# Performance work log

Measured on AMD Instinct MI355X. Metric: run time of the kernel, lower is better.

## Reference

```python
import jax, jax.numpy as jnp
import numpy as np

N_NODES = 50000
N_EDGES = 1600000
NODE_DIM = 1024
HID = 128
OUT = 128
LN_EPS = 1e-5


def setup_inputs() -> dict:
    key = jax.random.key(0)
    ks = jax.random.split(key, 8)
    s = lambda d: 1.0 / np.sqrt(d)
    return {
        "x": jax.random.normal(ks[0], (N_NODES, NODE_DIM), jnp.float32),
        "edge_index": jax.random.randint(ks[1], (2, N_EDGES), 0, N_NODES, jnp.int64),
        "proj_w": jax.random.normal(ks[2], (HID, NODE_DIM), jnp.float32) * s(NODE_DIM),
        "proj_b": jnp.zeros((HID,), jnp.float32),
        "lin_l_w": jax.random.normal(ks[3], (HID, HID), jnp.float32) * s(HID),
        "lin_l_b": jnp.zeros((HID,), jnp.float32),
        "lin_r_w": jax.random.normal(ks[4], (HID, HID), jnp.float32) * s(HID),
        "ln_g": jnp.ones((HID,), jnp.float32),
        "ln_b": jnp.zeros((HID,), jnp.float32),
        "out_w": jax.random.normal(ks[5], (OUT, HID), jnp.float32) * s(HID),
        "out_b": jnp.zeros((OUT,), jnp.float32),
    }


def reference(x, edge_index, proj_w, proj_b, lin_l_w, lin_l_b, lin_r_w, ln_g, ln_b, out_w, out_b):
    n = x.shape[0]
    # input projection + ReLU: [N, node_dim] -> [N, H]
    h = jax.nn.relu(x @ proj_w.T + proj_b)
    # SAGEConv(mean): gather source features, mean-scatter to targets
    src, dst = edge_index[0], edge_index[1]
    agg = jax.ops.segment_sum(h[src], dst, num_segments=n)  # [N, H]
    deg = jax.ops.segment_sum(jnp.ones((src.shape[0],), h.dtype), dst, num_segments=n)
    mean_nbr = agg / jnp.maximum(deg, 1.0)[:, None]
    h = mean_nbr @ lin_l_w.T + lin_l_b + h @ lin_r_w.T
    # LayerNorm over feature dim
    mu = h.mean(-1, keepdims=True)
    var = jnp.mean((h - mu) ** 2, -1, keepdims=True)
    h = (h - mu) * jax.lax.rsqrt(var + LN_EPS) * ln_g + ln_b
    h = jax.nn.relu(h)  # dropout is identity in eval
    # batch=None -> global mean pool over all nodes: [1, H]
    g = h.mean(0, keepdims=True)
    return g @ out_w.T + out_b
```

## Files before the change

kernel.cpp:

```cpp
#include <hip/hip_runtime.h>

#define N_NODES  50000
#define N_EDGES  1600000
#define NODE_DIM 1024
#define HID      128
#define LN_EPS   1e-5f
#define NBUCK    196
#define SHARD    6250

typedef float f32x4 __attribute__((ext_vector_type(4)));
typedef __bf16 bf16x8 __attribute__((ext_vector_type(8)));
typedef unsigned short u16x8 __attribute__((ext_vector_type(8)));
typedef unsigned int u32x4 __attribute__((ext_vector_type(4)));

__device__ __forceinline__ unsigned short f2bf(float f) {
  __bf16 b = (__bf16)f;
  return __builtin_bit_cast(unsigned short, b);
}
__device__ __forceinline__ unsigned int pkbf(float a, float b) {
  return (unsigned int)f2bf(a) | ((unsigned int)f2bf(b) << 16);
}
__device__ __forceinline__ float bf2f(unsigned short v) {
  return __uint_as_float((unsigned int)v << 16);
}

__device__ __forceinline__ int scan256_excl(int v, int buf[2][256], int t) {
  int cur = 0;
  buf[0][t] = v;
  __syncthreads();
  for (int off = 1; off < 256; off <<= 1) {
    int nxt = cur ^ 1;
    int s = buf[cur][t];
    if (t >= off) s += buf[cur][t - off];
    buf[nxt][t] = s;
    cur = nxt;
    __syncthreads();
  }
  return buf[cur][t] - v;
}

__global__ __launch_bounds__(256) void k_wpack(const float* __restrict__ w,
                                               unsigned short* __restrict__ wp) {
  int idx = blockIdx.x * 256 + threadIdx.x;
  int lane = idx & 63;
  int n = (idx >> 6) & 7;
  int ks = idx >> 9;
  int fr = lane & 15, kg = lane >> 4;
  const float* src = w + (size_t)(n * 16 + fr) * NODE_DIM + ks * 32 + kg * 8;
  float4 v0 = *(const float4*)(src);
  float4 v1 = *(const float4*)(src + 4);
  unsigned int* o = (unsigned int*)(wp + (size_t)idx * 8);
  o[0] = pkbf(v0.x, v0.y);
  o[1] = pkbf(v0.z, v0.w);
  o[2] = pkbf(v1.x, v1.y);
  o[3] = pkbf(v1.z, v1.w);
}

__global__ __launch_bounds__(256, 3) void k_proj(const float* __restrict__ x,
                                                 const unsigned short* __restrict__ wp,
                                                 const float* __restrict__ pb,
                                                 unsigned short* __restrict__ h) {
  const int wave = threadIdx.x >> 6, lane = threadIdx.x & 63;
  const int fr = lane & 15, kg = lane >> 4;
  const int strip = blockIdx.x * 4 + wave;
  const int m0 = strip * 32;

  int r0 = m0 + fr;      if (r0 >= N_NODES) r0 = N_NODES - 1;
  int r1 = m0 + 16 + fr; if (r1 >= N_NODES) r1 = N_NODES - 1;
  const float* a0p = x + (size_t)r0 * NODE_DIM + kg * 8;
  const float* a1p = x + (size_t)r1 * NODE_DIM + kg * 8;
  const bf16x8* bp = (const bf16x8*)wp + lane;

  f32x4 acc[2][8] = {};

  float4 xa0, xa1, xa2, xa3;
  float4 ya0, ya1, ya2, ya3;

#define LOADA_X(KS) { const float* p0 = a0p + (KS) * 32; const float* p1 = a1p + (KS) * 32; \
  xa0 = *(const float4*)p0; xa1 = *(const float4*)(p0 + 4); \
  xa2 = *(const float4*)p1; xa3 = *(const float4*)(p1 + 4); }
#define LOADA_Y(KS) { const float* p0 = a0p + (KS) * 32; const float* p1 = a1p + (KS) * 32; \
  ya0 = *(const float4*)p0; ya1 = *(const float4*)(p0 + 4); \
  ya2 = *(const float4*)p1; ya3 = *(const float4*)(p1 + 4); }

#define COMPUTE(A0, A1, A2, A3, KS) { \
  bf16x8 bfv[8]; \
  _Pragma("unroll") \
  for (int n = 0; n < 8; n++) bfv[n] = bp[((KS) * 8 + n) * 64]; \
  u32x4 pa0, pa1; \
  pa0[0] = pkbf(A0.x, A0.y); pa0[1] = pkbf(A0.z, A0.w); \
  pa0[2] = pkbf(A1.x, A1.y); pa0[3] = pkbf(A1.z, A1.w); \
  pa1[0] = pkbf(A2.x, A2.y); pa1[1] = pkbf(A2.z, A2.w); \
  pa1[2] = pkbf(A3.x, A3.y); pa1[3] = pkbf(A3.z, A3.w); \
  bf16x8 af0 = __builtin_bit_cast(bf16x8, pa0); \
  bf16x8 af1 = __builtin_bit_cast(bf16x8, pa1); \
  _Pragma("unroll") \
  for (int n = 0; n < 8; n++) { \
    acc[0][n] = __builtin_amdgcn_mfma_f32_16x16x32_bf16(af0, bfv[n], acc[0][n], 0, 0, 0); \
    acc[1][n] = __builtin_amdgcn_mfma_f32_16x16x32_bf16(af1, bfv[n], acc[1][n], 0, 0, 0); \
  } }

  LOADA_X(0);
  for (int ks = 0; ks < 32; ks += 2) {
    LOADA_Y(ks + 1);
    COMPUTE(xa0, xa1, xa2, xa3, ks);
    if (ks + 2 < 32) LOADA_X(ks + 2);
    COMPUTE(ya0, ya1, ya2, ya3, ks + 1);
  }
#undef LOADA_X
#undef LOADA_Y
#undef COMPUTE

  const int cr = (lane >> 4) * 4, cc = lane & 15;
#pragma unroll
  for (int n = 0; n < 8; n++) {
    const int col = n * 16 + cc;
    const float bias = pb[col];
#pragma unroll
    for (int m = 0; m < 2; m++) {
      const int rowb = m0 + m * 16 + cr;
#pragma unroll
      for (int i = 0; i < 4; i++) {
        float v = acc[m][n][i] + bias;
        h[(size_t)(rowb + i) * HID + col] = f2bf(v > 0.f ? v : 0.f);
      }
    }
  }
}

__global__ __launch_bounds__(256) void k_hist(const int* __restrict__ ei,
                                              int* __restrict__ counts) {
  __shared__ int bins[NBUCK];
  int t = threadIdx.x;
  if (t < NBUCK) bins[t] = 0;
  __syncthreads();
  int base = blockIdx.x * SHARD;
  for (int i = t; i < SHARD; i += 256)
    atomicAdd(&bins[ei[N_EDGES + base + i] >> 8], 1);
  __syncthreads();
  if (t < NBUCK) counts[t * 256 + blockIdx.x] = bins[t];
}

__global__ __launch_bounds__(256) void k_s1(const int* __restrict__ counts,
                                            int* __restrict__ basem,
                                            int* __restrict__ btot) {
  __shared__ int buf[2][256];
  int t = threadIdx.x, b = blockIdx.x;
  int v = counts[b * 256 + t];
  int excl = scan256_excl(v, buf, t);
  basem[b * 256 + t] = excl;
  if (t == 255) btot[b] = excl + v;
}

__global__ __launch_bounds__(256) void k_s2(const int* __restrict__ btot,
                                            int* __restrict__ bstart,
                                            float* __restrict__ accum) {
  __shared__ int buf[2][256];
  int t = threadIdx.x;
  int v = (t < NBUCK) ? btot[t] : 0;
  int excl = scan256_excl(v, buf, t);
  if (t < NBUCK) bstart[t] = excl;
  if (t == 0) bstart[NBUCK] = N_EDGES;
  if (t < HID) accum[t] = 0.f;
}

__global__ __launch_bounds__(256) void k_scatter(const int* __restrict__ ei,
                                                 const int* __restrict__ basem,
                                                 const int* __restrict__ bstart,
                                                 unsigned int* __restrict__ bs) {
  __shared__ int cur[NBUCK];
  int t = threadIdx.x;
  if (t < NBUCK) cur[t] = bstart[t] + basem[t * 256 + blockIdx.x];
  __syncthreads();
  int base = blockIdx.x * SHARD;
  for (int i = t; i < SHARD; i += 256) {
    int e = base + i;
    unsigned int src = (unsigned int)ei[e];
    unsigned int dst = (unsigned int)ei[N_EDGES + e];
    int pos = atomicAdd(&cur[dst >> 8], 1);
    bs[pos] = src | ((dst & 255u) << 16);
  }
}

__global__ __launch_bounds__(256) void k_bucket(const int* __restrict__ bstart,
                                                const unsigned int* __restrict__ bs,
                                                unsigned short* __restrict__ nbr,
                                                int* __restrict__ offs,
                                                int* __restrict__ deg) {
  __shared__ int bins[256];
  __shared__ int buf[2][256];
  __shared__ int curs[256];
  int t = threadIdx.x, b = blockIdx.x;
  int s = bstart[b], e = bstart[b + 1];
  bins[t] = 0;
  __syncthreads();
  for (int i = s + t; i < e; i += 256)
    atomicAdd(&bins[(bs[i] >> 16) & 255u], 1);
  __syncthreads();
  int v = bins[t];
  int excl = scan256_excl(v, buf, t);
  int node = b * 256 + t;
  deg[node]  = v;
  offs[node] = s + excl;
  curs[t]    = s + excl;
  __syncthreads();
  for (int i = s + t; i < e; i += 256) {
    unsigned int p = bs[i];
    int pos = atomicAdd(&curs[(p >> 16) & 255u], 1);
    nbr[pos] = (unsigned short)(p & 0xffffu);
  }
}

__global__ __launch_bounds__(256) void k_gather(const unsigned short* __restrict__ h,
                                                const unsigned short* __restrict__ nbr,
                                                const int* __restrict__ offs,
                                                const int* __restrict__ deg,
                                                unsigned short* __restrict__ mn) {
  const int wave = threadIdx.x >> 6;
  const int lane = threadIdx.x & 63;
  const int node = blockIdx.x * 4 + wave;
  if (node >= N_NODES) return;
  const int g = lane >> 4, li = lane & 15;
  const int d  = deg[node];
  const int st = offs[node];
  float a[8] = {0.f, 0.f, 0.f, 0.f, 0.f, 0.f, 0.f, 0.f};
  int n = g;
  for (; n + 4 < d; n += 8) {
    int s0 = nbr[st + n];
    int s1 = nbr[st + n + 4];
    u16x8 v0 = *(const u16x8*)(h + (size_t)s0 * HID + li * 8);
    u16x8 v1 = *(const u16x8*)(h + (size_t)s1 * HID + li * 8);
#pragma unroll
    for (int k = 0; k < 8; k++) a[k] += bf2f(v0[k]) + bf2f(v1[k]);
  }
  if (n < d) {
    int s0 = nbr[st + n];
    u16x8 v0 = *(const u16x8*)(h + (size_t)s0 * HID + li * 8);
#pragma unroll
    for (int k = 0; k < 8; k++) a[k] += bf2f(v0[k]);
  }
#pragma unroll
  for (int k = 0; k < 8; k++) {
    a[k] += __shfl_xor(a[k], 16);
    a[k] += __shfl_xor(a[k], 32);
  }
  if (g == 0) {
    float inv = 1.f / fmaxf((float)d, 1.f);
    u16x8 r;
#pragma unroll
    for (int k = 0; k < 8; k++) r[k] = f2bf(a[k] * inv);
    *(u16x8*)(mn + (size_t)node * HID + li * 8) = r;
  }
}

__global__ __launch_bounds__(256) void k_sage(const unsigned short* __restrict__ mn,
                                              const unsigned short* __restrict__ h,
                                              const float* __restrict__ wl,
                                              const float* __restrict__ wr,
                                              const float* __restrict__ lb,
                                              const float* __restrict__ lg,
                                              const float* __restrict__ lbt,
                                              float* __restrict__ accum) {
  __shared__ unsigned short As[128 * 32];
  __shared__ unsigned short Bs[128 * 32];
  __shared__ float T3[32 * 128];
  __shared__ float red[4][128];
  const int tid = threadIdx.x;
  const int m0 = blockIdx.x * 128;
  const int wave = tid >> 6, lane = tid & 63;
  const int wm = (wave >> 1) * 64, wn = (wave & 1) * 64;
  const int srow = tid >> 1, scol = (tid & 1) * 16;
  const int fr = lane & 15, ko = (lane >> 4) * 8;

  f32x4 acc[4][4] = {};

  for (int k0 = 0; k0 < 2 * HID; k0 += 32) {
    const unsigned short* baseA = (k0 < HID) ? mn : h;
    const float* baseB = (k0 < HID) ? wl : wr;
    const int kk = (k0 & (HID - 1)) + scol;
    const int arow = m0 + srow;
    u16x8 a0 = {0, 0, 0, 0, 0, 0, 0, 0}, a1 = a0;
    if (arow < N_NODES) {
      const u16x8* p = (const u16x8*)(baseA + (size_t)arow * HID + kk);
      a0 = p[0]; a1 = p[1];
    }
    const float4* q = (const float4*)(baseB + (size_t)srow * HID + kk);
    float4 b0 = q[0], b1 = q[1], b2 = q[2], b3 = q[3];

    __syncthreads();
    *(u16x8*)&As[srow * 32 + scol]     = a0;
    *(u16x8*)&As[srow * 32 + scol + 8] = a1;
    unsigned int* db = (unsigned int*)&Bs[srow * 32 + scol];
    db[0] = pkbf(b0.x, b0.y); db[1] = pkbf(b0.z, b0.w);
    db[2] = pkbf(b1.x, b1.y); db[3] = pkbf(b1.z, b1.w);
    db[4] = pkbf(b2.x, b2.y); db[5] = pkbf(b2.z, b2.w);
    db[6] = pkbf(b3.x, b3.y); db[7] = pkbf(b3.z, b3.w);
    __syncthreads();

    bf16x8 af[4], bfr[4];
#pragma unroll
    for (int m = 0; m < 4; m++)
      af[m] = *(const bf16x8*)&As[(wm + m * 16 + fr) * 32 + ko];
#pragma unroll
    for (int n = 0; n < 4; n++)
      bfr[n] = *(const bf16x8*)&Bs[(wn + n * 16 + fr) * 32 + ko];
#pragma unroll
    for (int m = 0; m < 4; m++)
#pragma unroll
      for (int n = 0; n < 4; n++)
        acc[m][n] = __builtin_amdgcn_mfma_f32_16x16x32_bf16(af[m], bfr[n], acc[m][n], 0, 0, 0);
  }

  const int cr = (lane >> 4) * 4, cc = lane & 15;
  const int p = wave >> 1;
  const float g0 = lg[lane], g1 = lg[lane + 64];
  const float t0 = lbt[lane], t1 = lbt[lane + 64];
  float ax = 0.f, ay = 0.f;
#pragma unroll
  for (int m = 0; m < 4; m++) {
    __syncthreads();
#pragma unroll
    for (int n = 0; n < 4; n++) {
      const int col = wn + n * 16 + cc;
      const float bias = lb[col];
#pragma unroll
      for (int i = 0; i < 4; i++)
        T3[(p * 16 + cr + i) * 128 + col] = acc[m][n][i] + bias;
    }
    __syncthreads();
    for (int r8 = 0; r8 < 8; r8++) {
      int q8 = wave * 8 + r8;
      int grow = m0 + (q8 >> 4) * 64 + m * 16 + (q8 & 15);
      float v0 = T3[q8 * 128 + lane];
      float v1 = T3[q8 * 128 + lane + 64];
      float sum = v0 + v1, ss = v0 * v0 + v1 * v1;
#pragma unroll
      for (int off = 32; off > 0; off >>= 1) {
        sum += __shfl_xor(sum, off);
        ss  += __shfl_xor(ss, off);
      }
      float mu  = sum * (1.f / HID);
      float var = ss * (1.f / HID) - mu * mu;
      float rinv = rsqrtf(var + LN_EPS);
      if (grow < N_NODES) {
        float y0 = (v0 - mu) * rinv * g0 + t0;
        float y1 = (v1 - mu) * rinv * g1 + t1;
        ax += fmaxf(y0, 0.f);
        ay += fmaxf(y1, 0.f);
      }
    }
  }
  red[wave][lane]      = ax;
  red[wave][lane + 64] = ay;
  __syncthreads();
  if (wave == 0) {
    float a  = red[0][lane] + red[1][lane] + red[2][lane] + red[3][lane];
    float bb = red[0][lane + 64] + red[1][lane + 64] + red[2][lane + 64] + red[3][lane + 64];
    atomicAdd(&accum[lane], a);
    atomicAdd(&accum[lane + 64], bb);
  }
}

__global__ __launch_bounds__(128) void k_final(const float* __restrict__ accum,
                                               const float* __restrict__ ow,
                                               const float* __restrict__ ob,
                                               float* __restrict__ out) {
  __shared__ float gs[HID];
  int t = threadIdx.x;
  gs[t] = accum[t] * (1.f / N_NODES);
  __syncthreads();
  float s = ob[t];
  for (int k = 0; k < HID; k++) s += gs[k] * ow[t * HID + k];
  out[t] = s;
}

extern "C" void kernel_launch(void* const* d_in, const int* in_sizes, int n_in,
                              void* d_out, int out_size, void* d_ws, size_t ws_size,
                              hipStream_t stream) {
  const float* x   = (const float*)d_in[0];
  const int*   ei  = (const int*)d_in[1];
  const float* pw  = (const float*)d_in[2];
  const float* pb  = (const float*)d_in[3];
  const float* wl  = (const float*)d_in[4];
  const float* lb  = (const float*)d_in[5];
  const float* wr  = (const float*)d_in[6];
  const float* lg  = (const float*)d_in[7];
  const float* lbt = (const float*)d_in[8];
  const float* ow  = (const float*)d_in[9];
  const float* ob  = (const float*)d_in[10];
  float* out = (float*)d_out;

  const int PAD = NBUCK * 256;
  unsigned short* h  = (unsigned short*)d_ws;
  unsigned short* mn = h + (size_t)PAD * HID;
  unsigned int* bsp  = (unsigned int*)(mn + (size_t)PAD * HID);
  unsigned short* nbr = (unsigned short*)(bsp + N_EDGES);
  int* counts = (int*)(nbr + N_EDGES);
  int* basem  = counts + NBUCK * 256;
  int* btot   = basem + NBUCK * 256;
  int* bstart = btot + 256;
  int* offs   = bstart + 256;
  int* deg    = offs + PAD;
  float* accum = (float*)(deg + PAD);
  unsigned short* wp = (unsigned short*)(accum + 128);

  const int MB  = (N_NODES + 127) / 128;
  const int PB  = (N_NODES + 127) / 128;
  (void)PB;

  hipLaunchKernelGGL(k_wpack,   dim3(64),    dim3(256), 0, stream, pw, wp);
  hipLaunchKernelGGL(k_hist,    dim3(256),   dim3(256), 0, stream, ei, counts);
  hipLaunchKernelGGL(k_s1,      dim3(NBUCK), dim3(256), 0, stream, counts, basem, btot);
  hipLaunchKernelGGL(k_s2,      dim3(1),     dim3(256), 0, stream, btot, bstart, accum);
  hipLaunchKernelGGL(k_scatter, dim3(256),   dim3(256), 0, stream, ei, basem, bstart, bsp);
  hipLaunchKernelGGL(k_bucket,  dim3(NBUCK), dim3(256), 0, stream, bstart, bsp, nbr, offs, deg);
  hipLaunchKernelGGL(k_proj,    dim3(392),   dim3(256), 0, stream, x, wp, pb, h);
  hipLaunchKernelGGL(k_gather,  dim3((N_NODES + 3) / 4), dim3(256), 0, stream, h, nbr, offs, deg, mn);
  hipLaunchKernelGGL(k_sage,    dim3(MB),    dim3(256), 0, stream, mn, h, wl, wr, lb, lg, lbt, accum);
  hipLaunchKernelGGL(k_final,   dim3(1),     dim3(128), 0, stream, accum, ow, ob, out);
}
```

Baseline: 473.6 us.

## Fuse all pipeline stages into one cooperative persistent kernel with grid syncs

Replaces the chain of separate launches (histogram, scans, scatter, bucket sort, projection, gather, SAGE/LayerNorm, final) with a single cooperative kernel of 512 blocks that runs the stages in sequence, separated by grid.sync(). Each stage loops over its original block indices with a grid stride. The aim is to remove per-launch overhead and the idle gaps between small kernels. The cost is that every phase is limited to 2 blocks per CU: the projection GEMM loses the occupancy of 3 it had before, and the grid-wide barriers add their own synchronisation cost. The accum zeroing moves into k_wpack, and the old multi-kernel path stays as a fallback if the cooperative launch fails.

```diff
diff --git a/kernel.cpp b/kernel.cpp
--- a/kernel.cpp
+++ b/kernel.cpp
@@ -1,4 +1,7 @@
 #include <hip/hip_runtime.h>
+#include <hip/hip_cooperative_groups.h>
+
+namespace cg = cooperative_groups;
 
 #define N_NODES  50000
 #define N_EDGES  1600000
@@ -7,6 +10,7 @@
 #define LN_EPS   1e-5f
 #define NBUCK    196
 #define SHARD    6250
+#define PSTRIPS  1568
 
 typedef float f32x4 __attribute__((ext_vector_type(4)));
 typedef __bf16 bf16x8 __attribute__((ext_vector_type(8)));
@@ -40,7 +44,9 @@
 }
 
 __global__ __launch_bounds__(256) void k_wpack(const float* __restrict__ w,
-                                               unsigned short* __restrict__ wp) {
+                                               unsigned short* __restrict__ wp,
+                                               float* __restrict__ accum) {
+  if (blockIdx.x == 0 && threadIdx.x < HID) accum[threadIdx.x] = 0.f;
   int idx = blockIdx.x * 256 + threadIdx.x;
   int lane = idx & 63;
   int n = (idx >> 6) & 7;
@@ -56,25 +62,20 @@
   o[3] = pkbf(v1.z, v1.w);
 }
 
-__global__ __launch_bounds__(256, 3) void k_proj(const float* __restrict__ x,
-                                                 const unsigned short* __restrict__ wp,
-                                                 const float* __restrict__ pb,
-                                                 unsigned short* __restrict__ h) {
-  const int wave = threadIdx.x >> 6, lane = threadIdx.x & 63;
+__device__ __forceinline__ void proj_strip(const float* __restrict__ x,
+                                           const unsigned short* __restrict__ wp,
+                                           const float* __restrict__ pb,
+                                           unsigned short* __restrict__ h,
+                                           int strip, int lane) {
   const int fr = lane & 15, kg = lane >> 4;
-  const int strip = blockIdx.x * 4 + wave;
-  const int m0 = strip * 32;
-
-  int r0 = m0 + fr;      if (r0 >= N_NODES) r0 = N_NODES - 1;
-  int r1 = m0 + 16 + fr; if (r1 >= N_NODES) r1 = N_NODES - 1;
+  const int m0s = strip * 32;
+  int r0 = m0s + fr;      if (r0 >= N_NODES) r0 = N_NODES - 1;
+  int r1 = m0s + 16 + fr; if (r1 >= N_NODES) r1 = N_NODES - 1;
   const float* a0p = x + (size_t)r0 * NODE_DIM + kg * 8;
   const float* a1p = x + (size_t)r1 * NODE_DIM + kg * 8;
   const bf16x8* bp = (const bf16x8*)wp + lane;
-
   f32x4 acc[2][8] = {};
-
-  float4 xa0, xa1, xa2, xa3;
-  float4 ya0, ya1, ya2, ya3;
+  float4 xa0, xa1, xa2, xa3, ya0, ya1, ya2, ya3;
 
 #define LOADA_X(KS) { const float* p0 = a0p + (KS) * 32; const float* p1 = a1p + (KS) * 32; \
   xa0 = *(const float4*)p0; xa1 = *(const float4*)(p0 + 4); \
@@ -82,7 +83,6 @@
 #define LOADA_Y(KS) { const float* p0 = a0p + (KS) * 32; const float* p1 = a1p + (KS) * 32; \
   ya0 = *(const float4*)p0; ya1 = *(const float4*)(p0 + 4); \
   ya2 = *(const float4*)p1; ya3 = *(const float4*)(p1 + 4); }
-
 #define COMPUTE(A0, A1, A2, A3, KS) { \
   bf16x8 bfv[8]; \
   _Pragma("unroll") \
@@ -118,7 +118,7 @@
     const float bias = pb[col];
 #pragma unroll
     for (int m = 0; m < 2; m++) {
-      const int rowb = m0 + m * 16 + cr;
+      const int rowb = m0s + m * 16 + cr;
 #pragma unroll
       for (int i = 0; i < 4; i++) {
         float v = acc[m][n][i] + bias;
@@ -126,6 +126,266 @@
       }
     }
   }
+}
+
+__global__ __launch_bounds__(256, 2) void k_mega(
+    const float* __restrict__ x, const int* __restrict__ ei,
+    const unsigned short* __restrict__ wp, const float* __restrict__ pb,
+    const float* __restrict__ wl, const float* __restrict__ lb,
+    const float* __restrict__ wr, const float* __restrict__ lg,
+    const float* __restrict__ lbt, const float* __restrict__ ow,
+    const float* __restrict__ ob,
+    unsigned short* __restrict__ h, unsigned short* __restrict__ mn,
+    unsigned int* __restrict__ bs, unsigned short* __restrict__ nbr,
+    int* __restrict__ counts, int* __restrict__ basem,
+    int* __restrict__ btot, int* __restrict__ bstart,
+    int* __restrict__ offs, int* __restrict__ deg,
+    float* __restrict__ accum, float* __restrict__ out) {
+  __shared__ __align__(16) unsigned char arena[18432];
+  const int tid = threadIdx.x;
+  const int wave = tid >> 6, lane = tid & 63;
+  const int nb = gridDim.x;
+  cg::grid_group grid = cg::this_grid();
+
+  {
+    int* bins = (int*)arena;
+    for (int vb = blockIdx.x; vb < 256; vb += nb) {
+      if (tid < NBUCK) bins[tid] = 0;
+      __syncthreads();
+      const int base = vb * SHARD;
+      for (int i = tid; i < SHARD; i += 256)
+        atomicAdd(&bins[ei[N_EDGES + base + i] >> 8], 1);
+      __syncthreads();
+      if (tid < NBUCK) counts[tid * 256 + vb] = bins[tid];
+      __syncthreads();
+    }
+  }
+  grid.sync();
+  {
+    int(*buf)[256] = (int(*)[256])arena;
+    for (int vb = blockIdx.x; vb < NBUCK; vb += nb) {
+      __syncthreads();
+      int v = counts[vb * 256 + tid];
+      int excl = scan256_excl(v, buf, tid);
+      basem[vb * 256 + tid] = excl;
+      if (tid == 255) btot[vb] = excl + v;
+    }
+  }
+  grid.sync();
+  if (blockIdx.x == 0) {
+    int(*buf)[256] = (int(*)[256])arena;
+    int v = (tid < NBUCK) ? btot[tid] : 0;
+    int excl = scan256_excl(v, buf, tid);
+    if (tid < NBUCK) bstart[tid] = excl;
+    if (tid == 0) bstart[NBUCK] = N_EDGES;
+  }
+  grid.sync();
+  {
+    int* cur = (int*)arena;
+    for (int vb = blockIdx.x; vb < 256; vb += nb) {
+      if (tid < NBUCK) cur[tid] = bstart[tid] + basem[tid * 256 + vb];
+      __syncthreads();
+      const int base = vb * SHARD;
+      for (int i = tid; i < SHARD; i += 256) {
+        int e = base + i;
+        unsigned int src = (unsigned int)ei[e];
+        unsigned int dst = (unsigned int)ei[N_EDGES + e];
+        int pos = atomicAdd(&cur[dst >> 8], 1);
+        bs[pos] = src | ((dst & 255u) << 16);
+      }
+      __syncthreads();
+    }
+  }
+  grid.sync();
+  {
+    int* bbins = (int*)arena;
+    int(*buf)[256] = (int(*)[256])(arena + 1024);
+    int* curs = (int*)(arena + 3072);
+    for (int q = blockIdx.x; q < NBUCK; q += nb) {
+      int s0 = bstart[q], e0 = bstart[q + 1];
+      __syncthreads();
+      bbins[tid] = 0;
+      __syncthreads();
+      for (int i = s0 + tid; i < e0; i += 256)
+        atomicAdd(&bbins[(bs[i] >> 16) & 255u], 1);
+      __syncthreads();
+      int v = bbins[tid];
+      int excl = scan256_excl(v, buf, tid);
+      int node = q * 256 + tid;
+      deg[node] = v;
+      offs[node] = s0 + excl;
+      curs[tid] = s0 + excl;
+      __syncthreads();
+      for (int i = s0 + tid; i < e0; i += 256) {
+        unsigned int p = bs[i];
+        int pos = atomicAdd(&curs[(p >> 16) & 255u], 1);
+        nbr[pos] = (unsigned short)(p & 0xffffu);
+      }
+    }
+  }
+  grid.sync();
+  for (int b4 = blockIdx.x; b4 < PSTRIPS / 4; b4 += nb)
+    proj_strip(x, wp, pb, h, b4 * 4 + wave, lane);
+  grid.sync();
+  {
+    const int g = lane >> 4, li = lane & 15;
+    const int nb4 = nb * 4;
+    for (int node = blockIdx.x * 4 + wave; node < N_NODES; node += nb4) {
+      const int d = deg[node];
+      const int st = offs[node];
+      float a[8] = {0.f, 0.f, 0.f, 0.f, 0.f, 0.f, 0.f, 0.f};
+      int n = g;
+      for (; n + 12 < d; n += 16) {
+        int s0 = nbr[st + n];
+        int s1 = nbr[st + n + 4];
+        int s2 = nbr[st + n + 8];
+        int s3 = nbr[st + n + 12];
+        u16x8 v0 = *(const u16x8*)(h + (size_t)s0 * HID + li * 8);
+        u16x8 v1 = *(const u16x8*)(h + (size_t)s1 * HID + li * 8);
+        u16x8 v2 = *(const u16x8*)(h + (size_t)s2 * HID + li * 8);
+        u16x8 v3 = *(const u16x8*)(h + (size_t)s3 * HID + li * 8);
+#pragma unroll
+        for (int k = 0; k < 8; k++)
+          a[k] += (bf2f(v0[k]) + bf2f(v1[k])) + (bf2f(v2[k]) + bf2f(v3[k]));
+      }
+      for (; n < d; n += 4) {
+        int s0 = nbr[st + n];
+        u16x8 v0 = *(const u16x8*)(h + (size_t)s0 * HID + li * 8);
+#pragma unroll
+        for (int k = 0; k < 8; k++) a[k] += bf2f(v0[k]);
+      }
+#pragma unroll
+      for (int k = 0; k < 8; k++) {
+        a[k] += __shfl_xor(a[k], 16);
+        a[k] += __shfl_xor(a[k], 32);
+      }
+      if (g == 0) {
+        float inv = 1.f / fmaxf((float)d, 1.f);
+        u16x8 r;
+#pragma unroll
+        for (int k = 0; k < 8; k++) r[k] = f2bf(a[k] * inv);
+        *(u16x8*)(mn + (size_t)node * HID + li * 8) = r;
+      }
+    }
+  }
+  grid.sync();
+  {
+    unsigned short* As = (unsigned short*)arena;
+    unsigned short* Bs = (unsigned short*)(arena + 8192);
+    float* T3 = (float*)arena;
+    float* red = (float*)(arena + 16384);
+    const int wm = (wave >> 1) * 64, wn = (wave & 1) * 64;
+    const int srow = tid >> 1, scol = (tid & 1) * 16;
+    const int sfr = lane & 15, sko = (lane >> 4) * 8;
+    const int cr = (lane >> 4) * 4, cc = lane & 15;
+    const int pq = wave >> 1;
+    const float g0 = lg[lane], g1 = lg[lane + 64];
+    const float t0 = lbt[lane], t1 = lbt[lane + 64];
+    const int nt = (N_NODES + 127) / 128;
+    for (int tile = blockIdx.x; tile < nt; tile += nb) {
+      const int m0 = tile * 128;
+      f32x4 acc[4][4] = {};
+      for (int k0 = 0; k0 < 2 * HID; k0 += 32) {
+        const unsigned short* baseA = (k0 < HID) ? mn : h;
+        const float* baseB = (k0 < HID) ? wl : wr;
+        const int kk = (k0 & (HID - 1)) + scol;
+        const int arow = m0 + srow;
+        u16x8 a0v = {0, 0, 0, 0, 0, 0, 0, 0}, a1v = a0v;
+        if (arow < N_NODES) {
+          const u16x8* p = (const u16x8*)(baseA + (size_t)arow * HID + kk);
+          a0v = p[0]; a1v = p[1];
+        }
+        const float4* q4 = (const float4*)(baseB + (size_t)srow * HID + kk);
+        float4 b0 = q4[0], b1 = q4[1], b2 = q4[2], b3 = q4[3];
+        __syncthreads();
+        *(u16x8*)&As[srow * 32 + scol] = a0v;
+        *(u16x8*)&As[srow * 32 + scol + 8] = a1v;
+        unsigned int* db = (unsigned int*)&Bs[srow * 32 + scol];
+        db[0] = pkbf(b0.x, b0.y); db[1] = pkbf(b0.z, b0.w);
+        db[2] = pkbf(b1.x, b1.y); db[3] = pkbf(b1.z, b1.w);
+        db[4] = pkbf(b2.x, b2.y); db[5] = pkbf(b2.z, b2.w);
+        db[6] = pkbf(b3.x, b3.y); db[7] = pkbf(b3.z, b3.w);
+        __syncthreads();
+        bf16x8 af[4], bfr[4];
+#pragma unroll
+        for (int m = 0; m < 4; m++)
+          af[m] = *(const bf16x8*)&As[(wm + m * 16 + sfr) * 32 + sko];
+#pragma unroll
+        for (int n2 = 0; n2 < 4; n2++)
+          bfr[n2] = *(const bf16x8*)&Bs[(wn + n2 * 16 + sfr) * 32 + sko];
+#pragma unroll
+        for (int m = 0; m < 4; m++)
+#pragma unroll
+          for (int n2 = 0; n2 < 4; n2++)
+            acc[m][n2] = __builtin_amdgcn_mfma_f32_16x16x32_bf16(af[m], bfr[n2], acc[m][n2], 0, 0, 0);
+      }
+      float ax = 0.f, ay = 0.f;
+#pragma unroll
+      for (int m = 0; m < 4; m++) {
+        __syncthreads();
+#pragma unroll
+        for (int n2 = 0; n2 < 4; n2++) {
+          const int col = wn + n2 * 16 + cc;
+          const float bias = lb[col];
+#pragma unroll
+          for (int i = 0; i < 4; i++)
+            T3[(pq * 16 + cr + i) * 128 + col] = acc[m][n2][i] + bias;
+        }
+        __syncthreads();
+        for (int r8 = 0; r8 < 8; r8++) {
+          int q8 = wave * 8 + r8;
+          int grow = m0 + (q8 >> 4) * 64 + m * 16 + (q8 & 15);
+          float v0 = T3[q8 * 128 + lane];
+          float v1 = T3[q8 * 128 + lane + 64];
+          float sum = v0 + v1, ss = v0 * v0 + v1 * v1;
+#pragma unroll
+          for (int off = 32; off > 0; off >>= 1) {
+            sum += __shfl_xor(sum, off);
+            ss += __shfl_xor(ss, off);
+          }
+          float mu = sum * (1.f / HID);
+          float var = ss * (1.f / HID) - mu * mu;
+          float rinv = rsqrtf(var + LN_EPS);
+          if (grow < N_NODES) {
+            float y0 = (v0 - mu) * rinv * g0 + t0;
+            float y1 = (v1 - mu) * rinv * g1 + t1;
+            ax += fmaxf(y0, 0.f);
+            ay += fmaxf(y1, 0.f);
+          }
+        }
+      }
+      red[wave * 128 + lane] = ax;
+      red[wave * 128 + lane + 64] = ay;
+      __syncthreads();
+      if (wave == 0) {
+        float aa = red[0 * 128 + lane] + red[1 * 128 + lane] +
+                   red[2 * 128 + lane] + red[3 * 128 + lane];
+        float bb = red[0 * 128 + lane + 64] + red[1 * 128 + lane + 64] +
+                   red[2 * 128 + lane + 64] + red[3 * 128 + lane + 64];
+        atomicAdd(&accum[lane], aa);
+        atomicAdd(&accum[lane + 64], bb);
+      }
+      __syncthreads();
+    }
+  }
+  grid.sync();
+  if (blockIdx.x == 0) {
+    float* gs = (float*)arena;
+    if (tid < HID) gs[tid] = accum[tid] * (1.f / N_NODES);
+    __syncthreads();
+    if (tid < HID) {
+      float s = ob[tid];
+      for (int k = 0; k < HID; k++) s += gs[k] * ow[tid * HID + k];
+      out[tid] = s;
+    }
+  }
+}
+
+__global__ __launch_bounds__(256, 3) void k_proj(const float* __restrict__ x,
+                                                 const unsigned short* __restrict__ wp,
+                                                 const float* __restrict__ pb,
+                                                 unsigned short* __restrict__ h) {
+  proj_strip(x, wp, pb, h, blockIdx.x * 4 + (threadIdx.x >> 6), threadIdx.x & 63);
 }
 
 __global__ __launch_bounds__(256) void k_hist(const int* __restrict__ ei,
@@ -404,18 +664,40 @@
   float* accum = (float*)(deg + PAD);
   unsigned short* wp = (unsigned short*)(accum + 128);
 
-  const int MB  = (N_NODES + 127) / 128;
-  const int PB  = (N_NODES + 127) / 128;
-  (void)PB;
-
-  hipLaunchKernelGGL(k_wpack,   dim3(64),    dim3(256), 0, stream, pw, wp);
-  hipLaunchKernelGGL(k_hist,    dim3(256),   dim3(256), 0, stream, ei, counts);
-  hipLaunchKernelGGL(k_s1,      dim3(NBUCK), dim3(256), 0, stream, counts, basem, btot);
-  hipLaunchKernelGGL(k_s2,      dim3(1),     dim3(256), 0, stream, btot, bstart, accum);
-  hipLaunchKernelGGL(k_scatter, dim3(256),   dim3(256), 0, stream, ei, basem, bstart, bsp);
-  hipLaunchKernelGGL(k_bucket,  dim3(NBUCK), dim3(256), 0, stream, bstart, bsp, nbr, offs, deg);
-  hipLaunchKernelGGL(k_proj,    dim3(392),   dim3(256), 0, stream, x, wp, pb, h);
-  hipLaunchKernelGGL(k_gather,  dim3((N_NODES + 3) / 4), dim3(256), 0, stream, h, nbr, offs, deg, mn);
-  hipLaunchKernelGGL(k_sage,    dim3(MB),    dim3(256), 0, stream, mn, h, wl, wr, lb, lg, lbt, accum);
-  hipLaunchKernelGGL(k_final,   dim3(1),     dim3(128), 0, stream, accum, ow, ob, out);
-}
+  hipLaunchKernelGGL(k_wpack, dim3(64), dim3(256), 0, stream, pw, wp, accum);
+
+  static int coop_grid = -1;
+  if (coop_grid < 0) {
+    int occ = 0;
+    hipError_t oe = hipOccupancyMaxActiveBlocksPerMultiprocessor(&occ, k_mega, 256, 0);
+    coop_grid = (oe == hipSuccess && occ >= 1) ? ((occ >= 2 ? 2 : 1) * 256) : 0;
+  }
+
+  bool done = false;
+  if (coop_grid > 0) {
+    void* kargs[] = {
+      (void*)&x, (void*)&ei, (void*)&wp, (void*)&pb, (void*)&wl, (void*)&lb,
+      (void*)&wr, (void*)&lg, (void*)&lbt, (void*)&ow, (void*)&ob,
+      (void*)&h, (void*)&mn, (void*)&bsp, (void*)&nbr,
+      (void*)&counts, (void*)&basem, (void*)&btot, (void*)&bstart,
+      (void*)&offs, (void*)&deg, (void*)&accum, (void*)&out
+    };
+    hipError_t err = hipLaunchCooperativeKernel((void*)k_mega, dim3(coop_grid),
+                                                dim3(256), kargs, 0, stream);
+    done = (err == hipSuccess);
+    if (!done) coop_grid = 0;
+  }
+
+  if (!done) {
+    const int MB = (N_NODES + 127) / 128;
+    hipLaunchKernelGGL(k_hist,    dim3(256),   dim3(256), 0, stream, ei, counts);
+    hipLaunchKernelGGL(k_s1,      dim3(NBUCK), dim3(256), 0, stream, counts, basem, btot);
+    hipLaunchKernelGGL(k_s2,      dim3(1),     dim3(256), 0, stream, btot, bstart, accum);
+    hipLaunchKernelGGL(k_scatter, dim3(256),   dim3(256), 0, stream, ei, basem, bstart, bsp);
+    hipLaunchKernelGGL(k_bucket,  dim3(NBUCK), dim3(256), 0, stream, bstart, bsp, nbr, offs, deg);
+    hipLaunchKernelGGL(k_proj,    dim3(392),   dim3(256), 0, stream, x, wp, pb, h);
+    hipLaunchKernelGGL(k_gather,  dim3((N_NODES + 3) / 4), dim3(256), 0, stream, h, nbr, offs, deg, mn);
+    hipLaunchKernelGGL(k_sage,    dim3(MB),    dim3(256), 0, stream, mn, h, wl, wr, lb, lg, lbt, accum);
+    hipLaunchKernelGGL(k_final,   dim3(1),     dim3(128), 0, stream, accum, ow, ob, out);
+  }
+}
```

New measurement: 840.0 us. 77.3% more time.
